# Kernel tuning notes

Hardware: AMD Instinct MI355X
Metric: run time of the kernel (lower is better)

## Reference

```python
import jax, jax.numpy as jnp
import numpy as np

D_MODEL = 1024
NUM_HEADS = 16
D_K = D_MODEL // NUM_HEADS
TEMPERATURE = 1.0
EPS = 1e-6


def setup_inputs() -> dict:
    key = jax.random.key(0)
    ks = jax.random.split(key, 8)
    B, S, D, H = 2, 2048, D_MODEL, NUM_HEADS
    sc = 1.0 / np.sqrt(D)
    x = jax.random.normal(ks[0], (B, S, D), dtype=jnp.float32)
    Wq = jax.random.normal(ks[1], (D, D), dtype=jnp.float32) * sc
    Wk = jax.random.normal(ks[2], (D, D), dtype=jnp.float32) * sc
    Wv = jax.random.normal(ks[3], (D, D), dtype=jnp.float32) * sc
    Wo = jax.random.normal(ks[4], (D, D), dtype=jnp.float32) * sc
    bo = jnp.zeros((D,), dtype=jnp.float32)
    phase_scale = jnp.ones((H,), dtype=jnp.float32)
    # orthogonal init for entanglement matrix
    q, _ = np.linalg.qr(np.random.default_rng(0).normal(size=(H, H)))
    ent = jnp.asarray(q, dtype=jnp.float32)
    gamma = jnp.ones((D,), dtype=jnp.float32)
    beta = jnp.zeros((D,), dtype=jnp.float32)
    return {"x": x, "Wq": Wq, "Wk": Wk, "Wv": Wv, "Wo": Wo, "bo": bo,
            "phase_scale": phase_scale, "ent": ent, "gamma": gamma, "beta": beta}


def reference(x, Wq, Wk, Wv, Wo, bo, phase_scale, ent, gamma, beta):
    B, S, D = x.shape
    H, dk = NUM_HEADS, D_K
    # projections -> [B, H, S, dk]
    Q = (x @ Wq).reshape(B, S, H, dk).transpose(0, 2, 1, 3)
    K = (x @ Wk).reshape(B, S, H, dk).transpose(0, 2, 1, 3)
    V = (x @ Wv).reshape(B, S, H, dk).transpose(0, 2, 1, 3)
    # per-head QK^T, scaled, phase-modulated
    scores = jnp.einsum('bhqd,bhkd->bhqk', Q, K)
    inv = 1.0 / (float(np.sqrt(dk)) * TEMPERATURE)
    s = scores * (inv * phase_scale)[None, :, None, None]
    # real part of quantum phase: cos(s) + 0.1*cos(2s)  (imag part of V is zero,
    # so head_output = attended_real; the 0.1*attended_imag term vanishes)
    w = jnp.cos(s) + 0.1 * jnp.cos(2.0 * s)
    w = jax.nn.softmax(w, axis=-1)
    att = jnp.einsum('bhqk,bhkd->bhqd', w, V).transpose(0, 2, 1, 3)  # [B,S,H,dk]
    # faithful reproduction of tf.einsum('bsnd,hm->bsmd', ...): sums over n AND h
    att = jnp.einsum('bsnd,hm->bsmd', att, ent)
    out = att.reshape(B, S, D) @ Wo + bo
    r = out + x
    mu = jnp.mean(r, axis=-1, keepdims=True)
    var = jnp.mean(jnp.square(r - mu), axis=-1, keepdims=True)
    return gamma * (r - mu) * jax.lax.rsqrt(var + EPS) + beta
```

## Files before the change

### kernel.cpp

```cpp
#include <hip/hip_runtime.h>
#include <cstdint>
#include <cstddef>

#define S_LEN 2048
#define DMODEL 1024
#define NHEADS 16
#define DKH 64
#define MROWS 4096
#define BH_CNT 32

typedef __bf16 bf16x8 __attribute__((ext_vector_type(8)));
typedef __bf16 bf16x2 __attribute__((ext_vector_type(2)));
typedef float f32x4 __attribute__((ext_vector_type(4)));
typedef unsigned int u32x4 __attribute__((ext_vector_type(4)));
typedef unsigned int u32;
typedef unsigned short u16;

__device__ __forceinline__ u16 f2bfu(float f) {
  u32 u = __float_as_uint(f);
  return (u16)((u + 0x7FFFu + ((u >> 16) & 1u)) >> 16);
}

__device__ __forceinline__ float bf2f(u16 v) {
  return __uint_as_float((u32)v << 16);
}

__device__ __forceinline__ u32 pk_bf16(float a, float b) {
  bf16x2 v;
  v[0] = (__bf16)a;
  v[1] = (__bf16)b;
  return __builtin_bit_cast(u32, v);
}

__device__ __forceinline__ void pl32swap(u32& a, u32& b) {
#if __has_builtin(__builtin_amdgcn_permlane32_swap)
  auto r = __builtin_amdgcn_permlane32_swap((int)a, (int)b, false, false);
  a = (u32)r[0]; b = (u32)r[1];
#else
  asm volatile("v_permlane32_swap_b32 %0, %1" : "+v"(a), "+v"(b));
#endif
}
__device__ __forceinline__ void pl16swap(u32& a, u32& b) {
#if __has_builtin(__builtin_amdgcn_permlane16_swap)
  auto r = __builtin_amdgcn_permlane16_swap((int)a, (int)b, false, false);
  a = (u32)r[0]; b = (u32)r[1];
#else
  asm volatile("v_permlane16_swap_b32 %0, %1" : "+v"(a), "+v"(b));
#endif
}

__device__ __forceinline__ void gload16(void* lds, const void* g) {
  __builtin_amdgcn_global_load_lds(
      (const __attribute__((address_space(1))) void*)g,
      (__attribute__((address_space(3))) void*)lds, 16, 0, 0);
}

__global__ __launch_bounds__(256) void prep_all_k(const float* __restrict__ x,
    const float* __restrict__ Wq, const float* __restrict__ Wk,
    const float* __restrict__ Wv, const float* __restrict__ Wo,
    const float* __restrict__ ps, const float* __restrict__ ent,
    u16* __restrict__ xb, u16* __restrict__ Wb, float* __restrict__ Woeff) {
  __shared__ float tile[32][33];
  int bid = blockIdx.x;
  int t = threadIdx.x;
  if (bid < 4096) {
    int i = (bid * 256 + t) * 4;
    float4 v = *(const float4*)(x + i);
    *(uint2*)(xb + i) = make_uint2(pk_bf16(v.x, v.y), pk_bf16(v.z, v.w));
  } else if (bid < 7168) {
    int lb = bid - 4096;
    int sel = lb >> 10, rem = lb & 1023;
    int k0 = (rem & 31) * 32, c0 = (rem >> 5) * 32;
    const float* W = sel == 0 ? Wq : (sel == 1 ? Wk : Wv);
    int tx = t & 31, ty = t >> 5;
#pragma unroll
    for (int i = 0; i < 4; ++i)
      tile[ty + i * 8][tx] = W[(size_t)(k0 + ty + i * 8) * DMODEL + c0 + tx];
    __syncthreads();
#pragma unroll
    for (int i = 0; i < 4; ++i) {
      int row = ty + i * 8;
      float v = tile[tx][row];
      if (sel == 1) v *= 0.019894367886486918f * ps[(c0 + row) >> 6];
      Wb[(size_t)(sel * 1024 + c0 + row) * DMODEL + k0 + tx] = f2bfu(v);
    }
  } else {
    __shared__ float e[16];
    if (t < 16) {
      float s = 0.f;
#pragma unroll
      for (int h = 0; h < 16; ++h) s += ent[h * 16 + t];
      e[t] = s;
    }
    __syncthreads();
    int gid = (bid - 7168) * 256 + t;
    int d = gid >> 10, j = gid & 1023;
    float acc = 0.f;
#pragma unroll
    for (int m = 0; m < 16; ++m) acc += e[m] * Wo[(size_t)((m << 6) + d) * DMODEL + j];
    Woeff[(size_t)d * DMODEL + j] = acc;
  }
}

__global__ __launch_bounds__(512, 2) void gemm_qkv_k(const u16* __restrict__ xb,
    const u16* __restrict__ Wb, u16* __restrict__ Qb, u16* __restrict__ Kb,
    u16* __restrict__ Vt) {
  __shared__ __align__(16) u16 As[2][8192];
  __shared__ __align__(16) u16 Bs[2][8192];
  int bid = blockIdx.x;
  int xcd = bid & 7, wi = bid >> 3;
  int mt = (xcd >> 1) * 4 + (wi & 3);
  int nt = (xcd & 1) * 6 + (wi >> 2);
  int m0 = mt * 256, n0 = nt * 256;
  int tid = threadIdx.x;
  int lane = tid & 63, w = tid >> 6;
  int c = lane & 15, g = lane >> 4;
  int wr = w >> 2, wcn = w & 3;

  int r2 = tid >> 2, s2 = tid & 3;
  const u16* aS = xb + (size_t)(m0 + r2) * DMODEL + ((s2 ^ (r2 & 3)) * 8);
  const u16* bS = Wb + (size_t)(n0 + r2) * DMODEL + ((s2 ^ (r2 & 3)) * 8);

  int xorc = (g ^ (c & 3)) * 8;
  int aoff[8], boff[4];
#pragma unroll
  for (int mf = 0; mf < 8; ++mf) aoff[mf] = (wr * 128 + mf * 16 + c) * 32 + xorc;
#pragma unroll
  for (int nf = 0; nf < 4; ++nf) boff[nf] = (wcn * 64 + nf * 16 + c) * 32 + xorc;

  f32x4 acc[8][4];
#pragma unroll
  for (int i = 0; i < 8; ++i)
#pragma unroll
    for (int j = 0; j < 4; ++j) acc[i][j] = (f32x4){0.f, 0.f, 0.f, 0.f};

  auto stage = [&](int buf, int kt) {
    gload16(&As[buf][tid * 8], aS + kt);
    gload16(&As[buf][4096 + tid * 8], aS + 128 * DMODEL + kt);
    gload16(&Bs[buf][tid * 8], bS + kt);
    gload16(&Bs[buf][4096 + tid * 8], bS + 128 * DMODEL + kt);
  };
  auto compute = [&](const int off) {
    bf16x8 bfr[4];
#pragma unroll
    for (int nf = 0; nf < 4; ++nf) bfr[nf] = *(const bf16x8*)(&Bs[0][0] + off + boff[nf]);
#pragma unroll
    for (int mf = 0; mf < 8; ++mf) {
      bf16x8 af = *(const bf16x8*)(&As[0][0] + off + aoff[mf]);
#pragma unroll
      for (int nf = 0; nf < 4; ++nf)
        acc[mf][nf] = __builtin_amdgcn_mfma_f32_16x16x32_bf16(af, bfr[nf], acc[mf][nf], 0, 0, 0);
    }
  };

  stage(0, 0);
  __syncthreads();
  for (int kt = 0; kt < DMODEL; kt += 64) {
    stage(1, kt + 32);
    compute(0);
    __syncthreads();
    if (kt + 64 < DMODEL) stage(0, kt + 64);
    compute(8192);
    __syncthreads();
  }

  int sel = nt >> 2;
  int h0 = (nt & 3) * 4;
  int b = m0 >> 11, sbase = m0 & 2047;
  char* Ls = (char*)&As[0][0];
#pragma unroll
  for (int half = 0; half < 2; ++half) {
    if (wr == half) {
      if (sel == 2) {
#pragma unroll
        for (int mf = 0; mf < 8; ++mf)
#pragma unroll
          for (int nf = 0; nf < 4; ++nf) {
            int n = wcn * 64 + nf * 16 + c;
            int mh = mf * 16 + 4 * g;
            *(uint2*)(Ls + n * 256 + ((mh * 2) ^ ((n & 7) << 4))) =
                make_uint2(pk_bf16(acc[mf][nf][0], acc[mf][nf][1]),
                           pk_bf16(acc[mf][nf][2], acc[mf][nf][3]));
          }
      } else {
#pragma unroll
        for (int mf = 0; mf < 8; ++mf)
#pragma unroll
          for (int nf = 0; nf < 4; ++nf) {
            int n = wcn * 64 + nf * 16 + c;
#pragma unroll
            for (int j = 0; j < 4; ++j) {
              int mh = mf * 16 + 4 * g + j;
              __bf16 hv = (__bf16)acc[mf][nf][j];
              *(u16*)(Ls + mh * 512 + ((n * 2) ^ ((mh & 7) << 4))) =
                  __builtin_bit_cast(u16, hv);
            }
          }
      }
    }
    __syncthreads();
    if (sel == 2) {
      int n = tid >> 1, cc = tid & 1;
      int head = h0 + (n >> 6), d = n & 63;
      u16* dst = Vt + ((size_t)(b * 16 + head) * DKH + d) * S_LEN + sbase + half * 128 + cc * 64;
#pragma unroll
      for (int kk = 0; kk < 8; ++kk)
        *(uint4*)(dst + kk * 8) =
            *(const uint4*)(Ls + n * 256 + ((cc * 128 + kk * 16) ^ ((n & 7) << 4)));
    } else {
      int r = tid >> 2, cc = tid & 3;
      int head = h0 + cc;
      u16* base = (sel == 0 ? Qb : Kb);
      u16* dst = base + ((size_t)(b * 16 + head) * S_LEN + sbase + half * 128 + r) * DKH;
#pragma unroll
      for (int kk = 0; kk < 8; ++kk)
        *(uint4*)(dst + kk * 8) =
            *(const uint4*)(Ls + r * 512 + ((cc * 128 + kk * 16) ^ ((r & 7) << 4)));
    }
    __syncthreads();
  }
}

__global__ __launch_bounds__(512) void attn_k(const u16* __restrict__ Qb,
    const u16* __restrict__ Kb, const u16* __restrict__ Vt,
    u16* __restrict__ attbufb) {
  __shared__ __align__(16) u16 Ks[4][4096];
  __shared__ __align__(16) u16 Vs[4][4096];
  __shared__ float dred[8][2][16];
  int fid = blockIdx.x;
  int swz = (fid & 7) * 64 + (fid >> 3);
  int bh = swz >> 4, qb = swz & 15;
  int tid = threadIdx.x;
  int lane = tid & 63, w = tid >> 6;
  int c = lane & 15, g = lane >> 4;
  int grp = w >> 2, h = (w >> 1) & 1, qh = w & 1;
  int q0 = qb * 128 + grp * 64;
  const float L2E = 1.4426950408889634f;

  const u16* Kbase = Kb + (size_t)bh * S_LEN * DKH;
  const u16* Vbase = Vt + (size_t)bh * DKH * S_LEN;

  int srow = w * 8 + (lane >> 3), slot = lane & 7, kp = slot ^ (srow & 7);
  const u16* kSrc = Kbase + (size_t)srow * DKH + kp * 8;
  const u16* vSrc = Vbase + (size_t)srow * S_LEN + kp * 8;
  auto stage = [&](int buf, int tile) {
    gload16(&Ks[buf][w * 512], kSrc + (size_t)tile * 64 * DKH);
    gload16(&Vs[buf][w * 512], vSrc + tile * 64);
  };

  int rot = qb * 2;
  stage(0, rot & 31);
  stage(1, (rot + 1) & 31);

  bf16x8 qf[2][2];
#pragma unroll
  for (int qg = 0; qg < 2; ++qg) {
    const u16* qp = Qb + ((size_t)bh * S_LEN + q0 + qh * 32 + qg * 16 + c) * DKH + g * 8;
    qf[qg][0] = *(const bf16x8*)qp;
    qf[qg][1] = *(const bf16x8*)(qp + 32);
  }
  bf16x8 onesf;
#pragma unroll
  for (int i = 0; i < 8; ++i) onesf[i] = (__bf16)1.0f;

  const u16* kptr[2][2];
#pragma unroll
  for (int fm = 0; fm < 2; ++fm) {
    int row = h * 32 + fm * 16 + c;
    kptr[fm][0] = &Ks[0][row * 64 + ((g ^ (row & 7)) * 8)];
    kptr[fm][1] = &Ks[0][row * 64 + (((4 + g) ^ (row & 7)) * 8)];
  }
  const u16* vptr[4];
#pragma unroll
  for (int fd = 0; fd < 4; ++fd) {
    int vrow = fd * 16 + c;
    vptr[fd] = &Vs[0][vrow * 64 + (((4 * h + g) ^ (vrow & 7)) * 8)];
  }

  f32x4 attT[4][2];
#pragma unroll
  for (int i = 0; i < 4; ++i)
#pragma unroll
    for (int qg = 0; qg < 2; ++qg) attT[i][qg] = (f32x4){0.f, 0.f, 0.f, 0.f};
  f32x4 denacc[2];
  denacc[0] = (f32x4){0.f, 0.f, 0.f, 0.f};
  denacc[1] = (f32x4){0.f, 0.f, 0.f, 0.f};

  auto compute = [&](const int off) {
    f32x4 sT[2][2];
    __builtin_amdgcn_s_setprio(1);
#pragma unroll
    for (int fm = 0; fm < 2; ++fm) {
      bf16x8 a0 = *(const bf16x8*)(kptr[fm][0] + off);
      bf16x8 a1 = *(const bf16x8*)(kptr[fm][1] + off);
#pragma unroll
      for (int qg = 0; qg < 2; ++qg) {
        f32x4 z = (f32x4){0.f, 0.f, 0.f, 0.f};
        z = __builtin_amdgcn_mfma_f32_16x16x32_bf16(a0, qf[qg][0], z, 0, 0, 0);
        sT[fm][qg] = __builtin_amdgcn_mfma_f32_16x16x32_bf16(a1, qf[qg][1], z, 0, 0, 0);
      }
    }
    __builtin_amdgcn_s_setprio(0);
    u32 wq[2][2][2];
#pragma unroll
    for (int fm = 0; fm < 2; ++fm)
#pragma unroll
      for (int qg = 0; qg < 2; ++qg) {
        float pv[4];
#pragma unroll
        for (int j = 0; j < 4; ++j) {
          float cv = __builtin_amdgcn_cosf(sT[fm][qg][j]);
          float w2 = __fmaf_rn(cv, __fmaf_rn(0.2f * L2E, cv, L2E), -0.1f * L2E);
          pv[j] = __builtin_amdgcn_exp2f(w2);
        }
        wq[qg][fm][0] = pk_bf16(pv[0], pv[1]);
        wq[qg][fm][1] = pk_bf16(pv[2], pv[3]);
      }
    bf16x8 pf[2];
#pragma unroll
    for (int qg = 0; qg < 2; ++qg) {
      u32 b0 = wq[qg][0][0], b2 = wq[qg][1][0];
      pl32swap(b0, b2);
      pl16swap(b0, b2);
      u32 b1 = wq[qg][0][1], b3 = wq[qg][1][1];
      pl32swap(b1, b3);
      pl16swap(b1, b3);
      pf[qg] = __builtin_bit_cast(bf16x8, (u32x4){b0, b1, b2, b3});
    }
    __builtin_amdgcn_s_setprio(1);
#pragma unroll
    for (int fd = 0; fd < 4; ++fd) {
      bf16x8 vf = *(const bf16x8*)(vptr[fd] + off);
#pragma unroll
      for (int qg = 0; qg < 2; ++qg)
        attT[fd][qg] = __builtin_amdgcn_mfma_f32_16x16x32_bf16(vf, pf[qg], attT[fd][qg], 0, 0, 0);
    }
#pragma unroll
    for (int qg = 0; qg < 2; ++qg)
      denacc[qg] = __builtin_amdgcn_mfma_f32_16x16x32_bf16(onesf, pf[qg], denacc[qg], 0, 0, 0);
    __builtin_amdgcn_s_setprio(0);
  };

  __syncthreads();
  for (int t = 0; t < 32; t += 4) {
    stage(2, (t + 2 + rot) & 31);
    stage(3, (t + 3 + rot) & 31);
    compute(0);
    compute(4096);
    __syncthreads();
    if (t + 4 < 32) {
      stage(0, (t + 4 + rot) & 31);
      stage(1, (t + 5 + rot) & 31);
    }
    compute(8192);
    compute(12288);
    __syncthreads();
  }

  if (g == 0) {
    dred[w][0][c] = denacc[0][0];
    dred[w][1][c] = denacc[1][0];
  }
  float* Rq = (grp ? (float*)&Vs[0][0] : (float*)&Ks[0][0]) + qh * 2048;
  if (h == 1) {
#pragma unroll
    for (int fd = 0; fd < 4; ++fd)
#pragma unroll
      for (int qg = 0; qg < 2; ++qg)
        *(f32x4*)&Rq[(qg * 16 + c) * 64 + fd * 16 + 4 * g] = attT[fd][qg];
  }
  __syncthreads();
  if (h == 0) {
    float inv[2];
#pragma unroll
    for (int qg = 0; qg < 2; ++qg)
      inv[qg] = 1.f / (dred[w][qg][c] + dred[w ^ 2][qg][c]);
#pragma unroll
    for (int fd = 0; fd < 4; ++fd)
#pragma unroll
      for (int qg = 0; qg < 2; ++qg) {
        f32x4 part = *(const f32x4*)&Rq[(qg * 16 + c) * 64 + fd * 16 + 4 * g];
        f32x4 tot = (attT[fd][qg] + part) * inv[qg];
        int q = q0 + qh * 32 + qg * 16 + c;
        *(uint2*)(attbufb + ((size_t)bh * S_LEN + q) * DKH + fd * 16 + 4 * g) =
            make_uint2(pk_bf16(tot[0], tot[1]), pk_bf16(tot[2], tot[3]));
      }
  }
}

__global__ __launch_bounds__(256) void fuse_out_ln_k(const u16* __restrict__ attbufb,
    const float* __restrict__ Woeff, const float* __restrict__ bo,
    const float* __restrict__ x, const float* __restrict__ gamma,
    const float* __restrict__ beta, float* __restrict__ out) {
  __shared__ float red[8][256];
  __shared__ __align__(16) float a[8][64];
  __shared__ float sred[8][4][2];
  int t = threadIdx.x;
  int r0 = blockIdx.x * 8;
  int d = t & 63, hg = t >> 6;
#pragma unroll
  for (int rr = 0; rr < 8; ++rr) {
    int m = r0 + rr, b = m >> 11, sr = m & 2047;
    float pa = 0.f;
#pragma unroll
    for (int hh = 0; hh < 4; ++hh) {
      int h = hg * 4 + hh;
      pa += bf2f(attbufb[(((size_t)(b * 16 + h)) * S_LEN + sr) * DKH + d]);
    }
    red[rr][t] = pa;
  }
  __syncthreads();
#pragma unroll
  for (int e = 0; e < 2; ++e) {
    int idx = t + e * 256;
    int rr = idx >> 6, dd = idx & 63;
    a[rr][dd] = red[rr][dd] + red[rr][64 + dd] + red[rr][128 + dd] + red[rr][192 + dd];
  }
  __syncthreads();

  float o[8][4];
#pragma unroll
  for (int rr = 0; rr < 8; ++rr) { o[rr][0] = o[rr][1] = o[rr][2] = o[rr][3] = 0.f; }
  int c4 = t * 4;
  for (int dd = 0; dd < 64; dd += 4) {
    float4 wv0 = *(const float4*)(Woeff + (size_t)(dd + 0) * DMODEL + c4);
    float4 wv1 = *(const float4*)(Woeff + (size_t)(dd + 1) * DMODEL + c4);
    float4 wv2 = *(const float4*)(Woeff + (size_t)(dd + 2) * DMODEL + c4);
    float4 wv3 = *(const float4*)(Woeff + (size_t)(dd + 3) * DMODEL + c4);
#pragma unroll
    for (int rr = 0; rr < 8; ++rr) {
      float4 av = *(const float4*)&a[rr][dd];
      o[rr][0] += av.x * wv0.x + av.y * wv1.x + av.z * wv2.x + av.w * wv3.x;
      o[rr][1] += av.x * wv0.y + av.y * wv1.y + av.z * wv2.y + av.w * wv3.y;
      o[rr][2] += av.x * wv0.z + av.y * wv1.z + av.z * wv2.z + av.w * wv3.z;
      o[rr][3] += av.x * wv0.w + av.y * wv1.w + av.z * wv2.w + av.w * wv3.w;
    }
  }
  float4 bv = *(const float4*)(bo + c4);
  int w = t >> 6, lane = t & 63;
#pragma unroll
  for (int rr = 0; rr < 8; ++rr) {
    int m = r0 + rr;
    float4 xv = *(const float4*)(x + (size_t)m * DMODEL + c4);
    o[rr][0] += bv.x + xv.x;
    o[rr][1] += bv.y + xv.y;
    o[rr][2] += bv.z + xv.z;
    o[rr][3] += bv.w + xv.w;
    float s = o[rr][0] + o[rr][1] + o[rr][2] + o[rr][3];
    float q = o[rr][0] * o[rr][0] + o[rr][1] * o[rr][1] + o[rr][2] * o[rr][2] + o[rr][3] * o[rr][3];
#pragma unroll
    for (int mm = 1; mm < 64; mm <<= 1) {
      s += __shfl_xor(s, mm, 64);
      q += __shfl_xor(q, mm, 64);
    }
    if (lane == 0) { sred[rr][w][0] = s; sred[rr][w][1] = q; }
  }
  __syncthreads();
  float4 gv = *(const float4*)(gamma + c4);
  float4 bev = *(const float4*)(beta + c4);
#pragma unroll
  for (int rr = 0; rr < 8; ++rr) {
    float s = sred[rr][0][0] + sred[rr][1][0] + sred[rr][2][0] + sred[rr][3][0];
    float q = sred[rr][0][1] + sred[rr][1][1] + sred[rr][2][1] + sred[rr][3][1];
    float mu = s * (1.f / 1024.f);
    float var = q * (1.f / 1024.f) - mu * mu;
    float rs = rsqrtf(var + 1e-6f);
    int m = r0 + rr;
    float4 ov;
    ov.x = gv.x * (o[rr][0] - mu) * rs + bev.x;
    ov.y = gv.y * (o[rr][1] - mu) * rs + bev.y;
    ov.z = gv.z * (o[rr][2] - mu) * rs + bev.z;
    ov.w = gv.w * (o[rr][3] - mu) * rs + bev.w;
    *(float4*)(out + (size_t)m * DMODEL + c4) = ov;
  }
}

extern "C" void kernel_launch(void* const* d_in, const int* in_sizes, int n_in,
                              void* d_out, int out_size, void* d_ws, size_t ws_size,
                              hipStream_t stream) {
  const float* x = (const float*)d_in[0];
  const float* Wq = (const float*)d_in[1];
  const float* Wk = (const float*)d_in[2];
  const float* Wv = (const float*)d_in[3];
  const float* Wo = (const float*)d_in[4];
  const float* bo = (const float*)d_in[5];
  const float* ps = (const float*)d_in[6];
  const float* ent = (const float*)d_in[7];
  const float* gamma = (const float*)d_in[8];
  const float* beta = (const float*)d_in[9];
  float* out = (float*)d_out;

  char* ws = (char*)d_ws;
  size_t o = 0;
  u16* xb = (u16*)(ws + o);    o += (size_t)MROWS * DMODEL * 2;
  u16* Wb = (u16*)(ws + o);    o += (size_t)3072 * 1024 * 2;
  u16* Qb = (u16*)(ws + o);    o += (size_t)BH_CNT * S_LEN * DKH * 2;
  u16* Kb = (u16*)(ws + o);    o += (size_t)BH_CNT * S_LEN * DKH * 2;
  u16* Vt = (u16*)(ws + o);    o += (size_t)BH_CNT * S_LEN * DKH * 2;
  float* Woeff = (float*)(ws + o);   o += (size_t)DKH * DMODEL * 4;
  u16* attbufb = (u16*)(ws + o);     o += (size_t)BH_CNT * S_LEN * DKH * 2;

  prep_all_k<<<dim3(7424), dim3(256), 0, stream>>>(x, Wq, Wk, Wv, Wo, ps, ent,
                                                   xb, Wb, Woeff);
  gemm_qkv_k<<<dim3(192), dim3(512), 0, stream>>>(xb, Wb, Qb, Kb, Vt);
  attn_k<<<dim3(512), dim3(512), 0, stream>>>(Qb, Kb, Vt, attbufb);
  fuse_out_ln_k<<<dim3(512), dim3(256), 0, stream>>>(attbufb, Woeff, bo, x, gamma, beta, out);
}
```

Baseline: 123.8 us.

## Halve attention query tile per block, double grid, shrink LDS to double buffer

Each attention block now handles 64 queries (16 per wave pair) instead of 128, so the grid doubles to 1024 blocks and each wave computes one 16-query group instead of two. The K/V staging pipeline drops from four to two shared-memory buffers, cutting LDS use, and the end-of-kernel reduction is adjusted to the new wave mapping. This targets occupancy and load balance across CUs. The cost is that every K/V tile is loaded twice as often overall, there is less MFMA work per LDS read, and there are more barriers per tile.

Result: slower. 129.3 us (+4.5%).

```diff
diff --git a/kernel.cpp b/kernel.cpp
--- a/kernel.cpp
+++ b/kernel.cpp
@@ -224,17 +224,17 @@
 __global__ __launch_bounds__(512) void attn_k(const u16* __restrict__ Qb,
     const u16* __restrict__ Kb, const u16* __restrict__ Vt,
     u16* __restrict__ attbufb) {
-  __shared__ __align__(16) u16 Ks[4][4096];
-  __shared__ __align__(16) u16 Vs[4][4096];
-  __shared__ float dred[8][2][16];
+  __shared__ __align__(16) u16 Ks[2][4096];
+  __shared__ __align__(16) u16 Vs[2][4096];
+  __shared__ float dred[8][16];
   int fid = blockIdx.x;
-  int swz = (fid & 7) * 64 + (fid >> 3);
-  int bh = swz >> 4, qb = swz & 15;
+  int swz = (fid & 7) * 128 + (fid >> 3);
+  int bh = swz >> 5, qb = swz & 31;
   int tid = threadIdx.x;
   int lane = tid & 63, w = tid >> 6;
   int c = lane & 15, g = lane >> 4;
-  int grp = w >> 2, h = (w >> 1) & 1, qh = w & 1;
-  int q0 = qb * 128 + grp * 64;
+  int h = w & 1, qq = w >> 1;
+  int q0 = qb * 64 + qq * 16;
   const float L2E = 1.4426950408889634f;
 
   const u16* Kbase = Kb + (size_t)bh * S_LEN * DKH;
@@ -248,16 +248,14 @@
     gload16(&Vs[buf][w * 512], vSrc + tile * 64);
   };
 
-  int rot = qb * 2;
+  int rot = qb;
   stage(0, rot & 31);
-  stage(1, (rot + 1) & 31);
-
-  bf16x8 qf[2][2];
-#pragma unroll
-  for (int qg = 0; qg < 2; ++qg) {
-    const u16* qp = Qb + ((size_t)bh * S_LEN + q0 + qh * 32 + qg * 16 + c) * DKH + g * 8;
-    qf[qg][0] = *(const bf16x8*)qp;
-    qf[qg][1] = *(const bf16x8*)(qp + 32);
+
+  bf16x8 qf[2];
+  {
+    const u16* qp = Qb + ((size_t)bh * S_LEN + q0 + c) * DKH + g * 8;
+    qf[0] = *(const bf16x8*)qp;
+    qf[1] = *(const bf16x8*)(qp + 32);
   }
   bf16x8 onesf;
 #pragma unroll
@@ -277,114 +275,81 @@
     vptr[fd] = &Vs[0][vrow * 64 + (((4 * h + g) ^ (vrow & 7)) * 8)];
   }
 
-  f32x4 attT[4][2];
-#pragma unroll
-  for (int i = 0; i < 4; ++i)
-#pragma unroll
-    for (int qg = 0; qg < 2; ++qg) attT[i][qg] = (f32x4){0.f, 0.f, 0.f, 0.f};
-  f32x4 denacc[2];
-  denacc[0] = (f32x4){0.f, 0.f, 0.f, 0.f};
-  denacc[1] = (f32x4){0.f, 0.f, 0.f, 0.f};
+  f32x4 attT[4];
+#pragma unroll
+  for (int i = 0; i < 4; ++i) attT[i] = (f32x4){0.f, 0.f, 0.f, 0.f};
+  f32x4 denacc = (f32x4){0.f, 0.f, 0.f, 0.f};
 
   auto compute = [&](const int off) {
-    f32x4 sT[2][2];
+    f32x4 sT[2];
     __builtin_amdgcn_s_setprio(1);
 #pragma unroll
     for (int fm = 0; fm < 2; ++fm) {
       bf16x8 a0 = *(const bf16x8*)(kptr[fm][0] + off);
       bf16x8 a1 = *(const bf16x8*)(kptr[fm][1] + off);
-#pragma unroll
-      for (int qg = 0; qg < 2; ++qg) {
-        f32x4 z = (f32x4){0.f, 0.f, 0.f, 0.f};
-        z = __builtin_amdgcn_mfma_f32_16x16x32_bf16(a0, qf[qg][0], z, 0, 0, 0);
-        sT[fm][qg] = __builtin_amdgcn_mfma_f32_16x16x32_bf16(a1, qf[qg][1], z, 0, 0, 0);
+      f32x4 z = (f32x4){0.f, 0.f, 0.f, 0.f};
+      z = __builtin_amdgcn_mfma_f32_16x16x32_bf16(a0, qf[0], z, 0, 0, 0);
+      sT[fm] = __builtin_amdgcn_mfma_f32_16x16x32_bf16(a1, qf[1], z, 0, 0, 0);
+    }
+    __builtin_amdgcn_s_setprio(0);
+    u32 wq[2][2];
+#pragma unroll
+    for (int fm = 0; fm < 2; ++fm) {
+      float pv[4];
+#pragma unroll
+      for (int j = 0; j < 4; ++j) {
+        float cv = __builtin_amdgcn_cosf(sT[fm][j]);
+        float w2 = __fmaf_rn(cv, __fmaf_rn(0.2f * L2E, cv, L2E), -0.1f * L2E);
+        pv[j] = __builtin_amdgcn_exp2f(w2);
       }
-    }
-    __builtin_amdgcn_s_setprio(0);
-    u32 wq[2][2][2];
-#pragma unroll
-    for (int fm = 0; fm < 2; ++fm)
-#pragma unroll
-      for (int qg = 0; qg < 2; ++qg) {
-        float pv[4];
-#pragma unroll
-        for (int j = 0; j < 4; ++j) {
-          float cv = __builtin_amdgcn_cosf(sT[fm][qg][j]);
-          float w2 = __fmaf_rn(cv, __fmaf_rn(0.2f * L2E, cv, L2E), -0.1f * L2E);
-          pv[j] = __builtin_amdgcn_exp2f(w2);
-        }
-        wq[qg][fm][0] = pk_bf16(pv[0], pv[1]);
-        wq[qg][fm][1] = pk_bf16(pv[2], pv[3]);
-      }
-    bf16x8 pf[2];
-#pragma unroll
-    for (int qg = 0; qg < 2; ++qg) {
-      u32 b0 = wq[qg][0][0], b2 = wq[qg][1][0];
-      pl32swap(b0, b2);
-      pl16swap(b0, b2);
-      u32 b1 = wq[qg][0][1], b3 = wq[qg][1][1];
-      pl32swap(b1, b3);
-      pl16swap(b1, b3);
-      pf[qg] = __builtin_bit_cast(bf16x8, (u32x4){b0, b1, b2, b3});
-    }
+      wq[fm][0] = pk_bf16(pv[0], pv[1]);
+      wq[fm][1] = pk_bf16(pv[2], pv[3]);
+    }
+    u32 b0 = wq[0][0], b2 = wq[1][0];
+    pl32swap(b0, b2);
+    pl16swap(b0, b2);
+    u32 b1 = wq[0][1], b3 = wq[1][1];
+    pl32swap(b1, b3);
+    pl16swap(b1, b3);
+    bf16x8 pf = __builtin_bit_cast(bf16x8, (u32x4){b0, b1, b2, b3});
     __builtin_amdgcn_s_setprio(1);
 #pragma unroll
     for (int fd = 0; fd < 4; ++fd) {
       bf16x8 vf = *(const bf16x8*)(vptr[fd] + off);
-#pragma unroll
-      for (int qg = 0; qg < 2; ++qg)
-        attT[fd][qg] = __builtin_amdgcn_mfma_f32_16x16x32_bf16(vf, pf[qg], attT[fd][qg], 0, 0, 0);
-    }
-#pragma unroll
-    for (int qg = 0; qg < 2; ++qg)
-      denacc[qg] = __builtin_amdgcn_mfma_f32_16x16x32_bf16(onesf, pf[qg], denacc[qg], 0, 0, 0);
+      attT[fd] = __builtin_amdgcn_mfma_f32_16x16x32_bf16(vf, pf, attT[fd], 0, 0, 0);
+    }
+    denacc = __builtin_amdgcn_mfma_f32_16x16x32_bf16(onesf, pf, denacc, 0, 0, 0);
     __builtin_amdgcn_s_setprio(0);
   };
 
   __syncthreads();
-  for (int t = 0; t < 32; t += 4) {
-    stage(2, (t + 2 + rot) & 31);
-    stage(3, (t + 3 + rot) & 31);
+  for (int t = 0; t < 32; t += 2) {
+    stage(1, (t + 1 + rot) & 31);
     compute(0);
+    __syncthreads();
+    if (t + 2 < 32) stage(0, (t + 2 + rot) & 31);
     compute(4096);
     __syncthreads();
-    if (t + 4 < 32) {
-      stage(0, (t + 4 + rot) & 31);
-      stage(1, (t + 5 + rot) & 31);
-    }
-    compute(8192);
-    compute(12288);
-    __syncthreads();
-  }
-
-  if (g == 0) {
-    dred[w][0][c] = denacc[0][0];
-    dred[w][1][c] = denacc[1][0];
-  }
-  float* Rq = (grp ? (float*)&Vs[0][0] : (float*)&Ks[0][0]) + qh * 2048;
+  }
+
+  if (g == 0) dred[w][c] = denacc[0];
+  float* Rq = (float*)&Ks[0][0] + qq * 1024;
   if (h == 1) {
 #pragma unroll
     for (int fd = 0; fd < 4; ++fd)
-#pragma unroll
-      for (int qg = 0; qg < 2; ++qg)
-        *(f32x4*)&Rq[(qg * 16 + c) * 64 + fd * 16 + 4 * g] = attT[fd][qg];
+      *(f32x4*)&Rq[c * 64 + fd * 16 + 4 * g] = attT[fd];
   }
   __syncthreads();
   if (h == 0) {
-    float inv[2];
-#pragma unroll
-    for (int qg = 0; qg < 2; ++qg)
-      inv[qg] = 1.f / (dred[w][qg][c] + dred[w ^ 2][qg][c]);
-#pragma unroll
-    for (int fd = 0; fd < 4; ++fd)
-#pragma unroll
-      for (int qg = 0; qg < 2; ++qg) {
-        f32x4 part = *(const f32x4*)&Rq[(qg * 16 + c) * 64 + fd * 16 + 4 * g];
-        f32x4 tot = (attT[fd][qg] + part) * inv[qg];
-        int q = q0 + qh * 32 + qg * 16 + c;
-        *(uint2*)(attbufb + ((size_t)bh * S_LEN + q) * DKH + fd * 16 + 4 * g) =
-            make_uint2(pk_bf16(tot[0], tot[1]), pk_bf16(tot[2], tot[3]));
-      }
+    float inv = 1.f / (dred[w][c] + dred[w ^ 1][c]);
+#pragma unroll
+    for (int fd = 0; fd < 4; ++fd) {
+      f32x4 part = *(const f32x4*)&Rq[c * 64 + fd * 16 + 4 * g];
+      f32x4 tot = (attT[fd] + part) * inv;
+      int q = q0 + c;
+      *(uint2*)(attbufb + ((size_t)bh * S_LEN + q) * DKH + fd * 16 + 4 * g) =
+          make_uint2(pk_bf16(tot[0], tot[1]), pk_bf16(tot[2], tot[3]));
+    }
   }
 }
 
@@ -503,6 +468,6 @@
   prep_all_k<<<dim3(7424), dim3(256), 0, stream>>>(x, Wq, Wk, Wv, Wo, ps, ent,
                                                    xb, Wb, Woeff);
   gemm_qkv_k<<<dim3(192), dim3(512), 0, stream>>>(xb, Wb, Qb, Kb, Vt);
-  attn_k<<<dim3(512), dim3(512), 0, stream>>>(Qb, Kb, Vt, attbufb);
+  attn_k<<<dim3(1024), dim3(512), 0, stream>>>(Qb, Kb, Vt, attbufb);
   fuse_out_ln_k<<<dim3(512), dim3(256), 0, stream>>>(attbufb, Woeff, bo, x, gamma, beta, out);
 }
```
